# Performance work log

Hardware: AMD Instinct MI355X
Metric: run time of the kernel (lower is better)

Reference implementation:

```python
import jax, jax.numpy as jnp
import numpy as np
from functools import partial

SEQ, BATCH, IN, HID = 512, 128, 256, 1024


def setup_inputs() -> dict:
    key = jax.random.key(0)
    ks = jax.random.split(key, 8)
    std = 1.0 / np.sqrt(HID)
    u = lambda k, shape: jax.random.uniform(k, shape, jnp.float32, -std, std)
    return {
        "inp": jax.random.normal(ks[0], (SEQ, BATCH, IN), jnp.float32),
        "Wxh": u(ks[1], (4 * HID, IN)),
        "bxh": u(ks[2], (4 * HID,)),
        "Whh": u(ks[3], (4 * HID, HID)),
        "bhh": u(ks[4], (4 * HID,)),
        "Wout": u(ks[5], (IN, HID)),
        "bout": u(ks[6], (IN,)),
    }


def lstm_forward(inp, Wxh, bxh, Whh, bhh, Wout, bout):
    seq, batch, _ = inp.shape
    hid = Whh.shape[1]
    # Precompute input projection for all timesteps: [T, B, 4H]
    x_proj = jnp.einsum("tbi,gi->tbg", inp, Wxh) + bxh

    def step(carry, xp_t):
        h, c = carry
        gates = xp_t + h @ Whh.T + bhh            # [B, 4H]
        i, f, g, o = jnp.split(gates, 4, axis=-1)  # torch chunk order: i,f,g,o
        c = jax.nn.sigmoid(f) * c + jax.nn.sigmoid(i) * jnp.tanh(g)
        h = jax.nn.sigmoid(o) * jnp.tanh(c)
        return (h, c), h

    h0 = jnp.zeros((batch, hid), inp.dtype)
    c0 = jnp.zeros((batch, hid), inp.dtype)
    _, hs = jax.lax.scan(step, (h0, c0), x_proj)   # hs: [T, B, H]
    out = jnp.einsum("tbh,ih->tbi", hs, Wout) + bout
    return jax.nn.log_softmax(out, axis=-1)


def reference(inp, Wxh, bxh, Whh, bhh, Wout, bout):
    return lstm_forward(inp, Wxh, bxh, Whh, bhh, Wout, bout)
```

## Files before the change

### kernel.cpp

```cpp
#include <hip/hip_runtime.h>
#include <math.h>


#define TT  512
#define BB  128
#define NIN 256
#define NH  1024
#define G4  4096
#define KK  1280
#define NBLK 160

typedef __bf16 bf16_t;
typedef bf16_t bf16x8 __attribute__((ext_vector_type(8)));
typedef float  f32x4  __attribute__((ext_vector_type(4)));

#define MFMA(a, b, c) __builtin_amdgcn_mfma_f32_16x16x32_bf16((a), (b), (c), 0, 0, 0)


__global__ void conv_w_kernel(const float* __restrict__ Wxh,
                              const float* __restrict__ Whh,
                              bf16_t* __restrict__ Wc) {
  const int n = blockIdx.y;
  const int k = blockIdx.x * 256 + threadIdx.x;
  const int g = n & 3, j = n >> 2;
  float v = (k < NIN) ? Wxh[(size_t)(g * NH + j) * NIN + k]
                      : Whh[(size_t)(g * NH + j) * NH + (k - NIN)];
  Wc[(size_t)n * KK + k] = (bf16_t)v;
}

__global__ void conv_f2b_kernel(const float* __restrict__ src,
                                bf16_t* __restrict__ dst, int n4) {
  int i = blockIdx.x * 256 + threadIdx.x;
  if (i < n4) {
    float4 v = ((const float4*)src)[i];
    dst[i * 4 + 0] = (bf16_t)v.x;
    dst[i * 4 + 1] = (bf16_t)v.y;
    dst[i * 4 + 2] = (bf16_t)v.z;
    dst[i * 4 + 3] = (bf16_t)v.w;
  }
}

__global__ void prep_bias_kernel(const float* __restrict__ bxh,
                                 const float* __restrict__ bhh,
                                 float* __restrict__ bsum4) {
  int n = blockIdx.x * 256 + threadIdx.x;
  int g = n & 3, j = n >> 2;
  bsum4[n] = bxh[g * NH + j] + bhh[g * NH + j];
}


__global__ __launch_bounds__(512) void lstm_persist(
    const bf16_t* __restrict__ x_bf,
    const bf16_t* __restrict__ Wc,
    const float*  __restrict__ bsum4,
    bf16_t*       __restrict__ hb0,
    bf16_t*       __restrict__ hb1,
    float*        __restrict__ cbuf,
    const bf16_t* __restrict__ WoutB,
    const float*  __restrict__ bout,
    float*        __restrict__ lgb0,
    float*        __restrict__ lgb1,
    float*        __restrict__ out,
    int* barcnt,
    int* barep)
{
  const int blk  = blockIdx.x;
  const int tid  = threadIdx.x;
  const int lane = tid & 63;
  const int wv   = tid >> 6;
  const int l16  = lane & 15;
  const int lq   = lane >> 4;

  __shared__ float gs[2][64 * 68];
  __shared__ float red[2][2][4][4];

  const int mb    = (blk & 1) * 64;
  const int ns    = blk >> 1;
  const int nbase = ns * 64;
  const int wm = wv & 1, wn = (wv >> 1) & 1, kh = wv >> 2;
  const int m0 = mb + wm * 32;
  const int n0 = nbase + wn * 32;

  for (int t = 0; t <= TT + 1; ++t) {
    const bf16_t* h_cur  = (t & 1) ? hb1 : hb0;
    bf16_t*       h_next = (t & 1) ? hb0 : hb1;
    float*        lgw    = (t & 1) ? lgb1 : lgb0;
    const float*  lgr    = (t & 1) ? lgb0 : lgb1;

    if (blk < 128 && t < TT) {
      const bf16_t* ax  = x_bf + (size_t)t * BB * NIN + (size_t)(m0 + l16) * NIN + lq * 8;
      const bf16_t* ah  = h_cur + (size_t)(m0 + l16) * NH + lq * 8;
      const bf16_t* b0p = Wc + (size_t)(n0 + l16) * KK + lq * 8;
      const bf16_t* b1p = Wc + (size_t)(n0 + 16 + l16) * KK + lq * 8;

      f32x4 a00 = {0,0,0,0}, a01 = {0,0,0,0}, a10 = {0,0,0,0}, a11 = {0,0,0,0};

      if (kh == 0) {
#pragma unroll
        for (int kk = 0; kk < 8; ++kk) {
          bf16x8 r0 = *(const bf16x8*)(ax + kk * 32);
          bf16x8 r1 = *(const bf16x8*)(ax + 16 * NIN + kk * 32);
          bf16x8 b0 = *(const bf16x8*)(b0p + kk * 32);
          bf16x8 b1 = *(const bf16x8*)(b1p + kk * 32);
          a00 = MFMA(r0, b0, a00); a01 = MFMA(r0, b1, a01);
          a10 = MFMA(r1, b0, a10); a11 = MFMA(r1, b1, a11);
        }
#pragma unroll 6
        for (int kk = 0; kk < 12; ++kk) {
          bf16x8 r0 = *(const bf16x8*)(ah + kk * 32);
          bf16x8 r1 = *(const bf16x8*)(ah + 16 * NH + kk * 32);
          bf16x8 b0 = *(const bf16x8*)(b0p + NIN + kk * 32);
          bf16x8 b1 = *(const bf16x8*)(b1p + NIN + kk * 32);
          a00 = MFMA(r0, b0, a00); a01 = MFMA(r0, b1, a01);
          a10 = MFMA(r1, b0, a10); a11 = MFMA(r1, b1, a11);
        }
      } else {
#pragma unroll 5
        for (int kk = 12; kk < 32; ++kk) {
          bf16x8 r0 = *(const bf16x8*)(ah + kk * 32);
          bf16x8 r1 = *(const bf16x8*)(ah + 16 * NH + kk * 32);
          bf16x8 b0 = *(const bf16x8*)(b0p + NIN + kk * 32);
          bf16x8 b1 = *(const bf16x8*)(b1p + NIN + kk * 32);
          a00 = MFMA(r0, b0, a00); a01 = MFMA(r0, b1, a01);
          a10 = MFMA(r1, b0, a10); a11 = MFMA(r1, b1, a11);
        }
      }

      float* g = gs[kh];
#pragma unroll
      for (int r = 0; r < 4; ++r) {
        const int rr0 = wm * 32 + lq * 4 + r;
        g[rr0 * 68 + wn * 32 + l16]             = a00[r];
        g[rr0 * 68 + wn * 32 + 16 + l16]        = a01[r];
        g[(rr0 + 16) * 68 + wn * 32 + l16]      = a10[r];
        g[(rr0 + 16) * 68 + wn * 32 + 16 + l16] = a11[r];
      }
      __syncthreads();

      const int b_l = tid >> 3;
#pragma unroll
      for (int p = 0; p < 2; ++p) {
        const int jl = (tid & 7) + p * 8;
        const int j  = ns * 16 + jl;
        float4 g0 = *(const float4*)&gs[0][b_l * 68 + jl * 4];
        float4 g1 = *(const float4*)&gs[1][b_l * 68 + jl * 4];
        float4 bs = ((const float4*)bsum4)[j];
        const float gi = g0.x + g1.x + bs.x;
        const float gf = g0.y + g1.y + bs.y;
        const float gg = g0.z + g1.z + bs.z;
        const float go = g0.w + g1.w + bs.w;
        const float si = 1.f / (1.f + __expf(-gi));
        const float sf = 1.f / (1.f + __expf(-gf));
        const float so = 1.f / (1.f + __expf(-go));
        const size_t idx = (size_t)(mb + b_l) * NH + j;
        const float cn = sf * cbuf[idx] + si * tanhf(gg);
        cbuf[idx] = cn;
        h_next[idx] = (bf16_t)(so * tanhf(cn));
      }
    } else if (blk >= 128 && blk < 144 && t >= 1 && t <= TT) {
      const int gw  = (blk - 128) * 8 + wv;
      const int bm0 = (gw >> 4) * 16;
      const int bn0 = (gw & 15) * 16;

      const bf16_t* ap = h_cur + (size_t)(bm0 + l16) * NH + lq * 8;
      const bf16_t* bp = WoutB + (size_t)(bn0 + l16) * NH + lq * 8;
      f32x4 acc = {0,0,0,0};
#pragma unroll 8
      for (int kk = 0; kk < 32; ++kk) {
        bf16x8 a = *(const bf16x8*)(ap + kk * 32);
        bf16x8 b = *(const bf16x8*)(bp + kk * 32);
        acc = MFMA(a, b, acc);
      }
      const float bo = bout[bn0 + l16];
#pragma unroll
      for (int r = 0; r < 4; ++r)
        lgw[(size_t)(bm0 + lq * 4 + r) * NIN + bn0 + l16] = acc[r] + bo;
    } else if (blk >= 144 && t >= 2) {
      const int sub  = tid >> 8;
      const int stid = tid & 255;
      const int swv  = (tid >> 6) & 3;
      const int b0 = (blk - 144) * 8 + sub * 4;
      float v[4], mx[4], sm[4];
#pragma unroll
      for (int r = 0; r < 4; ++r) v[r] = lgr[(size_t)(b0 + r) * NIN + stid];
#pragma unroll
      for (int r = 0; r < 4; ++r) mx[r] = v[r];
#pragma unroll
      for (int off = 32; off > 0; off >>= 1)
#pragma unroll
        for (int r = 0; r < 4; ++r) mx[r] = fmaxf(mx[r], __shfl_xor(mx[r], off));
      if (lane == 0)
#pragma unroll
        for (int r = 0; r < 4; ++r) red[0][sub][swv][r] = mx[r];
      __syncthreads();
#pragma unroll
      for (int r = 0; r < 4; ++r)
        mx[r] = fmaxf(fmaxf(red[0][sub][0][r], red[0][sub][1][r]),
                      fmaxf(red[0][sub][2][r], red[0][sub][3][r]));
#pragma unroll
      for (int r = 0; r < 4; ++r) sm[r] = __expf(v[r] - mx[r]);
#pragma unroll
      for (int off = 32; off > 0; off >>= 1)
#pragma unroll
        for (int r = 0; r < 4; ++r) sm[r] += __shfl_xor(sm[r], off);
      if (lane == 0)
#pragma unroll
        for (int r = 0; r < 4; ++r) red[1][sub][swv][r] = sm[r];
      __syncthreads();
      float* ot = out + (size_t)(t - 2) * BB * NIN + (size_t)b0 * NIN;
#pragma unroll
      for (int r = 0; r < 4; ++r) {
        float S = red[1][sub][0][r] + red[1][sub][1][r] +
                  red[1][sub][2][r] + red[1][sub][3][r];
        ot[(size_t)r * NIN + stid] = v[r] - mx[r] - logf(S);
      }
    }

    if (t <= TT) {
      const int ep = t + 1;
      __syncthreads();
      if (blk == 0) {
        if (tid < 8) {
          if (tid == 0) __threadfence();
          const int tgt = ((tid == 0) ? 19 : 20) * ep;
          int gcnt = 0;
          while (__hip_atomic_load(&barcnt[tid << 5], __ATOMIC_RELAXED,
                                   __HIP_MEMORY_SCOPE_AGENT) < tgt) {
            __builtin_amdgcn_s_sleep(1);
            if (++gcnt > (1 << 22)) break;
          }
        }
        __syncthreads();
        if (tid == 0) {
          __builtin_amdgcn_fence(__ATOMIC_ACQUIRE, "agent");
          __hip_atomic_store(barep, ep, __ATOMIC_RELEASE, __HIP_MEMORY_SCOPE_AGENT);
        }
        __syncthreads();
      } else {
        if (tid == 0) {
          __threadfence();
          __hip_atomic_fetch_add(&barcnt[(blk & 7) << 5], 1, __ATOMIC_RELAXED,
                                 __HIP_MEMORY_SCOPE_AGENT);
          int gcnt = 0;
          while (__hip_atomic_load(barep, __ATOMIC_RELAXED,
                                   __HIP_MEMORY_SCOPE_AGENT) < ep) {
            __builtin_amdgcn_s_sleep(1);
            if (++gcnt > (1 << 22)) break;
          }
          __builtin_amdgcn_fence(__ATOMIC_ACQUIRE, "agent");
        }
        __syncthreads();
      }
    }
  }
}


extern "C" void kernel_launch(void* const* d_in, const int* in_sizes, int n_in,
                              void* d_out, int out_size, void* d_ws, size_t ws_size,
                              hipStream_t stream) {
  const float* inp  = (const float*)d_in[0];
  const float* Wxh  = (const float*)d_in[1];
  const float* bxh  = (const float*)d_in[2];
  const float* Whh  = (const float*)d_in[3];
  const float* bhh  = (const float*)d_in[4];
  const float* Wout = (const float*)d_in[5];
  const float* boutp= (const float*)d_in[6];
  float* out = (float*)d_out;

  char* p = (char*)d_ws;
  bf16_t* Wc    = (bf16_t*)p; p += (size_t)G4 * KK * 2;
  bf16_t* x_bf  = (bf16_t*)p; p += (size_t)TT * BB * NIN * 2;
  bf16_t* WoutB = (bf16_t*)p; p += (size_t)NIN * NH * 2;
  bf16_t* h0    = (bf16_t*)p; p += (size_t)BB * NH * 2;
  bf16_t* h1    = (bf16_t*)p; p += (size_t)BB * NH * 2;
  float*  cbuf  = (float*)p;  p += (size_t)BB * NH * 4;
  float*  bsum4 = (float*)p;  p += (size_t)G4 * 4;
  float*  lg0   = (float*)p;  p += (size_t)BB * NIN * 4;
  float*  lg1   = (float*)p;  p += (size_t)BB * NIN * 4;
  int*    barcnt= (int*)p;    p += 8 * 32 * 4;
  int*    barep = (int*)p;    p += 32 * 4;

  conv_w_kernel<<<dim3(KK / 256, G4), 256, 0, stream>>>(Wxh, Whh, Wc);
  conv_f2b_kernel<<<(TT * BB * NIN / 4 + 255) / 256, 256, 0, stream>>>(
      inp, x_bf, TT * BB * NIN / 4);
  conv_f2b_kernel<<<(NIN * NH / 4 + 255) / 256, 256, 0, stream>>>(
      Wout, WoutB, NIN * NH / 4);
  prep_bias_kernel<<<G4 / 256, 256, 0, stream>>>(bxh, bhh, bsum4);
  hipMemsetAsync(h0, 0, (size_t)BB * NH * 2, stream);
  hipMemsetAsync(cbuf, 0, (size_t)BB * NH * 4, stream);
  hipMemsetAsync(barcnt, 0, (8 * 32 + 32) * 4, stream);

  lstm_persist<<<NBLK, 512, 0, stream>>>(
      x_bf, Wc, bsum4, h0, h1, cbuf, WoutB, boutp, lg0, lg1, out,
      barcnt, barep);
}
```

Measured before the change: 12.83 ms.

## Use flat grid barrier, register-resident cell state, and coherent atomic loads

Replaces the two-level grid barrier, where block 0 gathers the counters and then publishes an epoch, with a flat barrier in which every block increments a striped counter and spins on all eight counters. This removes one round trip per timestep. Memory fences are dropped, and cross-block visibility of h and the logits now relies on relaxed agent-scope atomic loads and stores that bypass non-coherent caches. The cell state c is kept in registers instead of a global buffer, and each thread's h pair is written as one packed 32-bit store. Without the fences, ordering between the atomic data stores and the barrier counter is less explicit, which is a correctness risk.

```diff
diff --git a/kernel.cpp b/kernel.cpp
--- a/kernel.cpp
+++ b/kernel.cpp
@@ -13,8 +13,30 @@
 typedef __bf16 bf16_t;
 typedef bf16_t bf16x8 __attribute__((ext_vector_type(8)));
 typedef float  f32x4  __attribute__((ext_vector_type(4)));
+typedef unsigned long long u64;
+typedef unsigned int u32;
+typedef unsigned short u16;
 
 #define MFMA(a, b, c) __builtin_amdgcn_mfma_f32_16x16x32_bf16((a), (b), (c), 0, 0, 0)
+
+__device__ __forceinline__ bf16x8 ldc16(const bf16_t* p) {
+  union { u64 q[2]; bf16x8 v; } u;
+  const u64* qp = (const u64*)p;
+  u.q[0] = __hip_atomic_load(qp,     __ATOMIC_RELAXED, __HIP_MEMORY_SCOPE_AGENT);
+  u.q[1] = __hip_atomic_load(qp + 1, __ATOMIC_RELAXED, __HIP_MEMORY_SCOPE_AGENT);
+  return u.v;
+}
+
+__device__ __forceinline__ float ldcf(const float* p) {
+  union { u32 i; float f; } u;
+  u.i = __hip_atomic_load((const u32*)p, __ATOMIC_RELAXED, __HIP_MEMORY_SCOPE_AGENT);
+  return u.f;
+}
+
+__device__ __forceinline__ void stcf(float* p, float v) {
+  union { u32 i; float f; } u; u.f = v;
+  __hip_atomic_store((u32*)p, u.i, __ATOMIC_RELAXED, __HIP_MEMORY_SCOPE_AGENT);
+}
 
 
 __global__ void conv_w_kernel(const float* __restrict__ Wxh,
@@ -55,14 +77,12 @@
     const float*  __restrict__ bsum4,
     bf16_t*       __restrict__ hb0,
     bf16_t*       __restrict__ hb1,
-    float*        __restrict__ cbuf,
     const bf16_t* __restrict__ WoutB,
     const float*  __restrict__ bout,
     float*        __restrict__ lgb0,
     float*        __restrict__ lgb1,
     float*        __restrict__ out,
-    int* barcnt,
-    int* barep)
+    int* barcnt)
 {
   const int blk  = blockIdx.x;
   const int tid  = threadIdx.x;
@@ -80,6 +100,10 @@
   const int wm = wv & 1, wn = (wv >> 1) & 1, kh = wv >> 2;
   const int m0 = mb + wm * 32;
   const int n0 = nbase + wn * 32;
+
+  const int b_l = tid >> 3;
+  const int j0l = (tid & 7) * 2;
+  float creg0 = 0.f, creg1 = 0.f;
 
   for (int t = 0; t <= TT + 1; ++t) {
     const bf16_t* h_cur  = (t & 1) ? hb1 : hb0;
@@ -107,8 +131,8 @@
         }
 #pragma unroll 6
         for (int kk = 0; kk < 12; ++kk) {
-          bf16x8 r0 = *(const bf16x8*)(ah + kk * 32);
-          bf16x8 r1 = *(const bf16x8*)(ah + 16 * NH + kk * 32);
+          bf16x8 r0 = ldc16(ah + kk * 32);
+          bf16x8 r1 = ldc16(ah + 16 * NH + kk * 32);
           bf16x8 b0 = *(const bf16x8*)(b0p + NIN + kk * 32);
           bf16x8 b1 = *(const bf16x8*)(b1p + NIN + kk * 32);
           a00 = MFMA(r0, b0, a00); a01 = MFMA(r0, b1, a01);
@@ -117,8 +141,8 @@
       } else {
 #pragma unroll 5
         for (int kk = 12; kk < 32; ++kk) {
-          bf16x8 r0 = *(const bf16x8*)(ah + kk * 32);
-          bf16x8 r1 = *(const bf16x8*)(ah + 16 * NH + kk * 32);
+          bf16x8 r0 = ldc16(ah + kk * 32);
+          bf16x8 r1 = ldc16(ah + 16 * NH + kk * 32);
           bf16x8 b0 = *(const bf16x8*)(b0p + NIN + kk * 32);
           bf16x8 b1 = *(const bf16x8*)(b1p + NIN + kk * 32);
           a00 = MFMA(r0, b0, a00); a01 = MFMA(r0, b1, a01);
@@ -137,10 +161,10 @@
       }
       __syncthreads();
 
-      const int b_l = tid >> 3;
+      u16 hbits[2];
 #pragma unroll
       for (int p = 0; p < 2; ++p) {
-        const int jl = (tid & 7) + p * 8;
+        const int jl = j0l + p;
         const int j  = ns * 16 + jl;
         float4 g0 = *(const float4*)&gs[0][b_l * 68 + jl * 4];
         float4 g1 = *(const float4*)&gs[1][b_l * 68 + jl * 4];
@@ -152,11 +176,16 @@
         const float si = 1.f / (1.f + __expf(-gi));
         const float sf = 1.f / (1.f + __expf(-gf));
         const float so = 1.f / (1.f + __expf(-go));
-        const size_t idx = (size_t)(mb + b_l) * NH + j;
-        const float cn = sf * cbuf[idx] + si * tanhf(gg);
-        cbuf[idx] = cn;
-        h_next[idx] = (bf16_t)(so * tanhf(cn));
-      }
+        const float cold = p ? creg1 : creg0;
+        const float cn = sf * cold + si * tanhf(gg);
+        if (p) creg1 = cn; else creg0 = cn;
+        union { bf16_t b; u16 u; } cv;
+        cv.b = (bf16_t)(so * tanhf(cn));
+        hbits[p] = cv.u;
+      }
+      const u32 packed = (u32)hbits[0] | ((u32)hbits[1] << 16);
+      u32* hp = (u32*)(h_next + (size_t)(mb + b_l) * NH + ns * 16 + j0l);
+      __hip_atomic_store(hp, packed, __ATOMIC_RELAXED, __HIP_MEMORY_SCOPE_AGENT);
     } else if (blk >= 128 && blk < 144 && t >= 1 && t <= TT) {
       const int gw  = (blk - 128) * 8 + wv;
       const int bm0 = (gw >> 4) * 16;
@@ -167,14 +196,14 @@
       f32x4 acc = {0,0,0,0};
 #pragma unroll 8
       for (int kk = 0; kk < 32; ++kk) {
-        bf16x8 a = *(const bf16x8*)(ap + kk * 32);
+        bf16x8 a = ldc16(ap + kk * 32);
         bf16x8 b = *(const bf16x8*)(bp + kk * 32);
         acc = MFMA(a, b, acc);
       }
       const float bo = bout[bn0 + l16];
 #pragma unroll
       for (int r = 0; r < 4; ++r)
-        lgw[(size_t)(bm0 + lq * 4 + r) * NIN + bn0 + l16] = acc[r] + bo;
+        stcf(&lgw[(size_t)(bm0 + lq * 4 + r) * NIN + bn0 + l16], acc[r] + bo);
     } else if (blk >= 144 && t >= 2) {
       const int sub  = tid >> 8;
       const int stid = tid & 255;
@@ -182,7 +211,7 @@
       const int b0 = (blk - 144) * 8 + sub * 4;
       float v[4], mx[4], sm[4];
 #pragma unroll
-      for (int r = 0; r < 4; ++r) v[r] = lgr[(size_t)(b0 + r) * NIN + stid];
+      for (int r = 0; r < 4; ++r) v[r] = ldcf(&lgr[(size_t)(b0 + r) * NIN + stid]);
 #pragma unroll
       for (int r = 0; r < 4; ++r) mx[r] = v[r];
 #pragma unroll
@@ -217,40 +246,21 @@
     }
 
     if (t <= TT) {
-      const int ep = t + 1;
-      __syncthreads();
-      if (blk == 0) {
-        if (tid < 8) {
-          if (tid == 0) __threadfence();
-          const int tgt = ((tid == 0) ? 19 : 20) * ep;
-          int gcnt = 0;
-          while (__hip_atomic_load(&barcnt[tid << 5], __ATOMIC_RELAXED,
-                                   __HIP_MEMORY_SCOPE_AGENT) < tgt) {
-            __builtin_amdgcn_s_sleep(1);
-            if (++gcnt > (1 << 22)) break;
-          }
+      const int tgt = 20 * (t + 1);
+      __syncthreads();
+      if (tid == 0)
+        __hip_atomic_fetch_add(&barcnt[(blk & 7) << 5], 1,
+                               __ATOMIC_RELAXED, __HIP_MEMORY_SCOPE_AGENT);
+      if (tid < 8) {
+        int gcnt = 0;
+        while (__hip_atomic_load(&barcnt[tid << 5], __ATOMIC_RELAXED,
+                                 __HIP_MEMORY_SCOPE_AGENT) < tgt) {
+          __builtin_amdgcn_s_sleep(1);
+          if (++gcnt > (1 << 24)) break;
         }
-        __syncthreads();
-        if (tid == 0) {
-          __builtin_amdgcn_fence(__ATOMIC_ACQUIRE, "agent");
-          __hip_atomic_store(barep, ep, __ATOMIC_RELEASE, __HIP_MEMORY_SCOPE_AGENT);
-        }
-        __syncthreads();
-      } else {
-        if (tid == 0) {
-          __threadfence();
-          __hip_atomic_fetch_add(&barcnt[(blk & 7) << 5], 1, __ATOMIC_RELAXED,
-                                 __HIP_MEMORY_SCOPE_AGENT);
-          int gcnt = 0;
-          while (__hip_atomic_load(barep, __ATOMIC_RELAXED,
-                                   __HIP_MEMORY_SCOPE_AGENT) < ep) {
-            __builtin_amdgcn_s_sleep(1);
-            if (++gcnt > (1 << 22)) break;
-          }
-          __builtin_amdgcn_fence(__ATOMIC_ACQUIRE, "agent");
-        }
-        __syncthreads();
-      }
+      }
+      asm volatile("" ::: "memory");
+      __syncthreads();
     }
   }
 }
@@ -274,12 +284,10 @@
   bf16_t* WoutB = (bf16_t*)p; p += (size_t)NIN * NH * 2;
   bf16_t* h0    = (bf16_t*)p; p += (size_t)BB * NH * 2;
   bf16_t* h1    = (bf16_t*)p; p += (size_t)BB * NH * 2;
-  float*  cbuf  = (float*)p;  p += (size_t)BB * NH * 4;
   float*  bsum4 = (float*)p;  p += (size_t)G4 * 4;
   float*  lg0   = (float*)p;  p += (size_t)BB * NIN * 4;
   float*  lg1   = (float*)p;  p += (size_t)BB * NIN * 4;
   int*    barcnt= (int*)p;    p += 8 * 32 * 4;
-  int*    barep = (int*)p;    p += 32 * 4;
 
   conv_w_kernel<<<dim3(KK / 256, G4), 256, 0, stream>>>(Wxh, Whh, Wc);
   conv_f2b_kernel<<<(TT * BB * NIN / 4 + 255) / 256, 256, 0, stream>>>(
@@ -288,10 +296,9 @@
       Wout, WoutB, NIN * NH / 4);
   prep_bias_kernel<<<G4 / 256, 256, 0, stream>>>(bxh, bhh, bsum4);
   hipMemsetAsync(h0, 0, (size_t)BB * NH * 2, stream);
-  hipMemsetAsync(cbuf, 0, (size_t)BB * NH * 4, stream);
-  hipMemsetAsync(barcnt, 0, (8 * 32 + 32) * 4, stream);
+  hipMemsetAsync(h1, 0, (size_t)BB * NH * 2, stream);
+  hipMemsetAsync(barcnt, 0, 8 * 32 * 4, stream);
 
   lstm_persist<<<NBLK, 512, 0, stream>>>(
-      x_bf, Wc, bsum4, h0, h1, cbuf, WoutB, boutp, lg0, lg1, out,
-      barcnt, barep);
-}
+      x_bf, Wc, bsum4, h0, h1, WoutB, boutp, lg0, lg1, out, barcnt);
+}
```

Result: slower. 13.96 ms (+8.8%).
